# Kernel tuning notes

Hardware: AMD Instinct MI355X
Metric: run time of the kernel (lower is better)

The kernel has to match this reference:

```python
import math
import jax, jax.numpy as jnp
import numpy as np
from jax import lax

B, L = 8192, 512          # batch, seq_len; configs.d_model == seq_len (forced by LayerNorm over last dim)
TREND_POLY = 3
F_LEN = L // 2 - 1        # rfft bins after slicing [low_freq=1 : -1] for even t
TOP_K = int(math.log(F_LEN))  # = 5


def setup_inputs() -> dict:
    key = jax.random.key(0)
    ks = jax.random.split(key, 12)
    s = 0.02
    return {
        "x": jax.random.normal(ks[0], (B, L, 1), dtype=jnp.float32),
        "conv1_w": jax.random.normal(ks[1], (TREND_POLY, 1, 3), dtype=jnp.float32) * s,
        "conv1_b": jnp.zeros((TREND_POLY,), dtype=jnp.float32),
        "conv3_w": jax.random.normal(ks[2], (L, L, 3), dtype=jnp.float32) * s,
        "conv3_b": jnp.zeros((L,), dtype=jnp.float32),
        "w1": jax.random.normal(ks[3], (L, L), dtype=jnp.float32) * s,
        "b1": jnp.zeros((L,), dtype=jnp.float32),
        "w2": jax.random.normal(ks[4], (L, L), dtype=jnp.float32) * s,
        "b2": jnp.zeros((L,), dtype=jnp.float32),
        "ln_g": jnp.ones((L,), dtype=jnp.float32),
        "ln_b": jnp.zeros((L,), dtype=jnp.float32),
    }


def _gelu(x):
    return jax.nn.gelu(x, approximate=False)  # torch nn.GELU default (erf)


def _conv1d(x, w, b):
    # x: (b, Cin, T), w: (Cout, Cin, 3), padding=1
    y = lax.conv_general_dilated(x, w, window_strides=(1,), padding=[(1, 1)],
                                 dimension_numbers=("NCH", "OIH", "NCH"))
    return y + b[None, :, None]


def _trend_block(xp, conv1_w, conv1_b, conv3_w, conv3_b):
    # xp: (b, 1, L)
    h = _gelu(_conv1d(xp, conv1_w, conv1_b))        # (b, 3, L)
    h = h.transpose(0, 2, 1)                         # (b, L, 3) -- channels = seq_len
    h = _conv1d(h, conv3_w, conv3_b)                 # (b, L, 3)
    # poly_space: lin_space = [1/(out_dim+1)] = [0.5]; powers 1..3 -> (3, 1)
    lin = jnp.array([0.5], dtype=xp.dtype)
    poly = jnp.stack([lin ** (p + 1) for p in range(TREND_POLY)], axis=0)  # (3,1)
    # torch: (b,L,3) @ (3,1) -> (b,L,1) -> transpose -> (b,1,L)
    return jnp.einsum("blp,po->bol", h, poly)        # (b, 1, L)


def _fourier_layer(x):
    # x: (b, t, d=1); low_freq=1, t even
    b, t, d = x.shape
    xf = jnp.fft.rfft(x, axis=1)[:, 1:-1]            # (b, F, d) complex
    freqs = jnp.fft.rfftfreq(t).astype(x.dtype)[1:-1]  # (F,)
    mag = jnp.abs(xf)                                # (b, F, d)
    _, idx = lax.top_k(mag.transpose(0, 2, 1), TOP_K)  # (b, d, k)
    idx = idx.transpose(0, 2, 1)                     # (b, k, d)
    xf_sel = jnp.take_along_axis(xf, idx, axis=1)    # (b, k, d)
    f_sel = freqs[idx]                               # (b, k, d)
    # extrapolate with conjugate-symmetric pairs
    xf2 = jnp.concatenate([xf_sel, jnp.conj(xf_sel)], axis=1)       # (b, 2k, d)
    f2 = jnp.concatenate([f_sel, -f_sel], axis=1)[:, :, None, :]    # (b, 2k, 1, d)
    tt = jnp.arange(t, dtype=x.dtype)[None, None, :, None]          # (1, 1, t, 1)
    amp = jnp.abs(xf2)[:, :, None, :]                               # (b, 2k, 1, d)
    phase = jnp.arctan2(xf2.imag, xf2.real)[:, :, None, :]
    x_time = amp * jnp.cos(2.0 * math.pi * f2 * tt + phase)         # (b, 2k, t, d)
    return jnp.sum(x_time, axis=1)                                  # (b, t, d)


def reference(x, conv1_w, conv1_b, conv3_w, conv3_b, w1, b1, w2, b2, ln_g, ln_b):
    xp = x.transpose(0, 2, 1)                        # (b, 1, L)
    trend = _trend_block(xp, conv1_w, conv1_b, conv3_w, conv3_b)    # (b, 1, L)
    season = _fourier_layer(x).transpose(0, 2, 1)    # (b, 1, L)
    # residual MLP branch on enc_out = (b, 1, L); LayerNorm over last dim (== d_model)
    e = xp
    mu = jnp.mean(e, axis=-1, keepdims=True)
    var = jnp.mean((e - mu) ** 2, axis=-1, keepdims=True)
    ln = (e - mu) * lax.rsqrt(var + 1e-5) * ln_g + ln_b
    m = _gelu(jnp.einsum("bcl,ol->bco", ln, w1) + b1)
    m = jnp.einsum("bcl,ol->bco", m, w2) + b2        # dropout is identity at eval
    e = e + m
    mean = jnp.mean(e, axis=1, keepdims=True)        # dim 1 has size 1 -> mean == e
    return (e - mean, season, trend, mean)
```

## Files before the change

### kernel.cpp

```cpp
#include <hip/hip_runtime.h>
#include <hip/hip_bf16.h>
#include <math.h>

#define B_ 8192
#define L_ 512
#define BL_ (B_ * L_)
#define KT_ 1536

using bf16x8 = __attribute__((ext_vector_type(8))) short;
using f32x4  = __attribute__((ext_vector_type(4))) float;

__device__ __forceinline__ float gelu_f(float v) {
    return 0.5f * v * (1.0f + erff(v * 0.70710678118654752f));
}
__device__ __forceinline__ float bf2f(unsigned short u) {
    return __uint_as_float(((unsigned int)u) << 16);
}
__device__ __forceinline__ unsigned short f2bf(float f) {
    unsigned int x = __float_as_uint(f);
    x += 0x7fffu + ((x >> 16) & 1u);
    return (unsigned short)(x >> 16);
}
__device__ __forceinline__ void gload16(const void* g, void* l) {
    __builtin_amdgcn_global_load_lds(
        (const __attribute__((address_space(1))) unsigned int*)g,
        (__attribute__((address_space(3))) unsigned int*)l, 16, 0, 0);
}

__global__ __launch_bounds__(256) void k_fused_pre(const float* __restrict__ x,
        const float* __restrict__ c1w, const float* __restrict__ c1b,
        const float* __restrict__ lg, const float* __restrict__ lbias,
        unsigned short* __restrict__ h1, unsigned short* __restrict__ lnx,
        const float* __restrict__ c3w, const float* __restrict__ w1,
        const float* __restrict__ w2, unsigned short* __restrict__ weff,
        unsigned short* __restrict__ w1b, unsigned short* __restrict__ w2b,
        double2* __restrict__ tabd, float2* __restrict__ tab,
        float2* __restrict__ tab32) {
    const int tid = threadIdx.x;
    if (blockIdx.x >= B_) {
        int idx = (blockIdx.x - B_) * 256 + tid;
        if (idx < 512) {
            double sv, cv;
            sincos((double)idx * (3.14159265358979323846 / 256.0), &sv, &cv);
            tabd[idx] = make_double2(cv, sv);
            tab[idx] = make_float2((float)cv, (float)sv);
            if ((idx & 15) == 0) tab32[idx >> 4] = make_float2((float)cv, (float)sv);
        }
        int o = idx >> 9, i = idx & 511;
        const float* t = c3w + (size_t)idx * 3;
        float t0 = t[0], t1 = t[1], t2 = t[2];
        size_t base = (size_t)o * KT_ + i;
        weff[base]        = f2bf(0.25f * t0 + 0.5f * t1);
        weff[base + 512]  = f2bf(0.125f * t0 + 0.25f * t1 + 0.5f * t2);
        weff[base + 1024] = f2bf(0.125f * t1 + 0.25f * t2);
        w1b[idx] = f2bf(w1[idx]);
        w2b[idx] = f2bf(w2[idx]);
        return;
    }
    __shared__ float xs[512];
    __shared__ float red[8];
    const long b = blockIdx.x;
    const float* xr = x + (b << 9);
    float x0 = xr[tid], x1 = xr[tid + 256];
    xs[tid] = x0; xs[tid + 256] = x1;
    float s = x0 + x1, ss = x0 * x0 + x1 * x1;
#pragma unroll
    for (int off = 32; off > 0; off >>= 1) {
        s += __shfl_xor(s, off);
        ss += __shfl_xor(ss, off);
    }
    if ((tid & 63) == 0) { red[tid >> 6] = s; red[4 + (tid >> 6)] = ss; }
    __syncthreads();
    s  = red[0] + red[1] + red[2] + red[3];
    ss = red[4] + red[5] + red[6] + red[7];
    const float mu = s * (1.f / 512.f);
    const float rs = rsqrtf(ss * (1.f / 512.f) - mu * mu + 1e-5f);
    float w[9], cb[3];
#pragma unroll
    for (int j = 0; j < 9; ++j) w[j] = c1w[j];
#pragma unroll
    for (int j = 0; j < 3; ++j) cb[j] = c1b[j];
#pragma unroll
    for (int half = 0; half < 2; ++half) {
        const int i = tid + (half << 8);
        const float xm = i ? xs[i - 1] : 0.f;
        const float xc = xs[i];
        const float xp = (i != 511) ? xs[i + 1] : 0.f;
        unsigned short* hb = h1 + b * KT_ + i;
#pragma unroll
        for (int c = 0; c < 3; ++c) {
            float v = w[c * 3] * xm + w[c * 3 + 1] * xc + w[c * 3 + 2] * xp + cb[c];
            hb[(long)c << 9] = f2bf(gelu_f(v));
        }
        lnx[(b << 9) + i] = f2bf(fmaf((xc - mu) * rs, lg[i], lbias[i]));
    }
}

template<int EMODE, int KD>
__global__ __launch_bounds__(256) void k_mgemm(
        const unsigned short* __restrict__ A, const unsigned short* __restrict__ W,
        const float* __restrict__ bias, float sbias,
        const float* __restrict__ xres, void* __restrict__ Cp) {
    __shared__ short As[128][64];
    __shared__ short Bs[64][64];
    const int tid = threadIdx.x;
    const int lane = tid & 63;
    const int wid = tid >> 6;
    const int m0 = blockIdx.x << 7;
    const int n0 = blockIdx.y << 6;
    const int wm = (wid & 1) << 6;
    const int wn = (wid >> 1) << 5;
    f32x4 acc[4][2] = {};

    const int srow = tid >> 3;
    const int schunk = tid & 7;
    const unsigned short* Ab = A + (size_t)m0 * KD;
    const unsigned short* Wb = W + (size_t)n0 * KD;
    const int frow = lane & 15;
    const int fsw = frow & 7;
    const int s0 = lane >> 4;

    for (int k0 = 0; k0 < KD; k0 += 64) {
        __syncthreads();
#pragma unroll
        for (int seg = 0; seg < 4; ++seg) {
            const int r = (seg << 5) + srow;
            const int c = (schunk ^ (r & 7)) << 3;
            gload16(Ab + (size_t)r * KD + k0 + c, &As[r][schunk << 3]);
        }
#pragma unroll
        for (int seg = 0; seg < 2; ++seg) {
            const int r = (seg << 5) + srow;
            const int c = (schunk ^ (r & 7)) << 3;
            gload16(Wb + (size_t)r * KD + k0 + c, &Bs[r][schunk << 3]);
        }
        __syncthreads();
#pragma unroll
        for (int kk = 0; kk < 2; ++kk) {
            bf16x8 af[4], bfr[2];
            const int sl = (kk << 2) + s0;
#pragma unroll
            for (int m = 0; m < 4; ++m)
                af[m] = *(const bf16x8*)&As[wm + (m << 4) + frow][(sl ^ fsw) << 3];
#pragma unroll
            for (int n = 0; n < 2; ++n)
                bfr[n] = *(const bf16x8*)&Bs[wn + (n << 4) + frow][(sl ^ fsw) << 3];
#pragma unroll
            for (int m = 0; m < 4; ++m)
#pragma unroll
                for (int n = 0; n < 2; ++n)
                    acc[m][n] = __builtin_amdgcn_mfma_f32_16x16x32_bf16(af[m], bfr[n], acc[m][n], 0, 0, 0);
        }
    }

    const int col0 = n0 + wn + (lane & 15);
    const int rbase = m0 + wm + ((lane >> 4) << 2);
#pragma unroll
    for (int n = 0; n < 2; ++n) {
        const int col = col0 + (n << 4);
        const float bz = sbias * bias[col];
#pragma unroll
        for (int m = 0; m < 4; ++m) {
#pragma unroll
            for (int r = 0; r < 4; ++r) {
                const size_t row = rbase + (m << 4) + r;
                float v = acc[m][n][r] + bz;
                if (EMODE == 0) {
                    ((float*)Cp)[row * 512 + col] = v;
                } else if (EMODE == 1) {
                    ((unsigned short*)Cp)[row * 512 + col] = f2bf(gelu_f(v));
                } else {
                    ((float*)Cp)[row * 512 + col] = v + xres[row * 512 + col];
                }
            }
        }
    }
}

__global__ __launch_bounds__(256) void k_season(const float* __restrict__ x,
        const double2* __restrict__ gtabd, const float2* __restrict__ gtab,
        const float2* __restrict__ gtab32,
        float* __restrict__ out1, float* __restrict__ out0) {
    __shared__ float2 xp[2][256];
    __shared__ float2 tab[512];
    __shared__ float2 Ys[2][512];
    __shared__ unsigned long long wkey[2][4][5];
    __shared__ float2 wval[2][4][5];

    const int tid = threadIdx.x;
    const int w = tid >> 6, l = tid & 63;
    const long b = (long)blockIdx.x << 1;
    const float* xr0 = x + (b << 9);
    const float* xr1 = xr0 + 512;

    {
        const int t1s = tid >> 3, t0s = tid & 7;
        const int g = (t1s << 4) + t0s;
        xp[0][tid] = make_float2(xr0[g], xr0[g + 8]);
        xp[1][tid] = make_float2(xr1[g], xr1[g + 8]);
        tab[tid] = gtab[tid];
        tab[tid + 256] = gtab[tid + 256];
    }
    __syncthreads();

    const int rr = (w << 3) + (l & 7);
    const int t0 = l >> 3;
    float ra0 = 0.f, ia0 = 0.f, rb0 = 0.f, ib0 = 0.f;
    float ra1 = 0.f, ia1 = 0.f, rb1 = 0.f, ib1 = 0.f;
    int e32 = 0;
#pragma unroll
    for (int t1 = 0; t1 < 32; ++t1) {
        float2 wt = gtab32[e32];
        e32 = (e32 + rr) & 31;
        float2 v0 = xp[0][(t1 << 3) + t0];
        float2 v1 = xp[1][(t1 << 3) + t0];
        ra0 = fmaf(v0.x, wt.x, ra0); ia0 = fmaf(v0.x, wt.y, ia0);
        rb0 = fmaf(v0.y, wt.x, rb0); ib0 = fmaf(v0.y, wt.y, ib0);
        ra1 = fmaf(v1.x, wt.x, ra1); ia1 = fmaf(v1.x, wt.y, ia1);
        rb1 = fmaf(v1.y, wt.x, rb1); ib1 = fmaf(v1.y, wt.y, ib1);
    }
    Ys[0][(t0 << 5) + rr] = make_float2(ra0, -ia0);
    Ys[0][((t0 + 8) << 5) + rr] = make_float2(rb0, -ib0);
    Ys[1][(t0 << 5) + rr] = make_float2(ra1, -ia1);
    Ys[1][((t0 + 8) << 5) + rr] = make_float2(rb1, -ib1);

    const int k = ((l >> 3) << 5) + rr;
    double xre0 = 0.0, xim0 = 0.0, xre1 = 0.0, xim1 = 0.0;
    int e = 0;
#pragma unroll
    for (int t0i = 0; t0i < 16; ++t0i) {
        float2 y0 = Ys[0][(t0i << 5) + rr];
        float2 y1 = Ys[1][(t0i << 5) + rr];
        double2 wt = gtabd[e];
        e = (e + k) & 511;
        xre0 += (double)y0.x * wt.x + (double)y0.y * wt.y;
        xim0 += (double)y0.y * wt.x - (double)y0.x * wt.y;
        xre1 += (double)y1.x * wt.x + (double)y1.y * wt.y;
        xim1 += (double)y1.y * wt.x - (double)y1.x * wt.y;
    }

    unsigned long long key0 = 0, key1 = 0;
    if (k != 0) {
        double m0 = xre0 * xre0 + xim0 * xim0;
        double m1 = xre1 * xre1 + xim1 * xim1;
        key0 = (__double_as_longlong(m0) & ~0xFFFull) | (unsigned long long)(4095 - k);
        key1 = (__double_as_longlong(m1) & ~0xFFFull) | (unsigned long long)(4095 - k);
    }
    const float fre0 = (float)xre0, fim0 = (float)xim0;
    const float fre1 = (float)xre1, fim1 = (float)xim1;

    for (int rnd = 0; rnd < 5; ++rnd) {
        unsigned long long rk0 = key0, rk1 = key1;
#pragma unroll
        for (int off = 32; off > 0; off >>= 1) {
            unsigned long long o0 = __shfl_xor(rk0, off);
            unsigned long long o1 = __shfl_xor(rk1, off);
            rk0 = (o0 > rk0) ? o0 : rk0;
            rk1 = (o1 > rk1) ? o1 : rk1;
        }
        if (key0 == rk0 && rk0 != 0ull) {
            wkey[0][w][rnd] = rk0; wval[0][w][rnd] = make_float2(fre0, fim0); key0 = 0;
        }
        if (key1 == rk1 && rk1 != 0ull) {
            wkey[1][w][rnd] = rk1; wval[1][w][rnd] = make_float2(fre1, fim1); key1 = 0;
        }
    }
    __syncthreads();

#pragma unroll
    for (int row = 0; row < 2; ++row) {
        float4 sel[5];
        int h0 = 0, h1 = 0, h2 = 0, h3 = 0;
#pragma unroll
        for (int rnd = 0; rnd < 5; ++rnd) {
            unsigned long long c0 = wkey[row][0][h0], c1 = wkey[row][1][h1];
            unsigned long long c2 = wkey[row][2][h2], c3 = wkey[row][3][h3];
            unsigned long long bk = c0; int bw = 0;
            if (c1 > bk) { bk = c1; bw = 1; }
            if (c2 > bk) { bk = c2; bw = 2; }
            if (c3 > bk) { bk = c3; bw = 3; }
            const int hs = (bw == 0) ? h0 : (bw == 1) ? h1 : (bw == 2) ? h2 : h3;
            float2 v = wval[row][bw][hs];
            h0 += (bw == 0); h1 += (bw == 1); h2 += (bw == 2); h3 += (bw == 3);
            const int kk = 4095 - (int)(bk & 0xFFFull);
            sel[rnd] = make_float4((float)kk, v.x, v.y, 0.f);
        }
        const long ro = ((b + row) << 9);
#pragma unroll
        for (int half = 0; half < 2; ++half) {
            int t = tid + (half << 8);
            float acc = 0.f;
#pragma unroll
            for (int j = 0; j < 5; ++j) {
                float4 sj = sel[j];
                int kj = (int)sj.x;
                float2 wt = tab[(kj * t) & 511];
                acc += sj.y * wt.x - sj.z * wt.y;
            }
            out1[ro + t] = 2.f * acc;
            out0[ro + t] = 0.f;
        }
    }
}

extern "C" void kernel_launch(void* const* d_in, const int* in_sizes, int n_in,
                              void* d_out, int out_size, void* d_ws, size_t ws_size,
                              hipStream_t stream) {
    const float* x   = (const float*)d_in[0];
    const float* c1w = (const float*)d_in[1];
    const float* c1b = (const float*)d_in[2];
    const float* c3w = (const float*)d_in[3];
    const float* c3b = (const float*)d_in[4];
    const float* w1  = (const float*)d_in[5];
    const float* b1  = (const float*)d_in[6];
    const float* w2  = (const float*)d_in[7];
    const float* b2  = (const float*)d_in[8];
    const float* lg  = (const float*)d_in[9];
    const float* lb  = (const float*)d_in[10];

    float* out  = (float*)d_out;
    float* out1 = out + (long)BL_;
    float* out2 = out + 2L * BL_;
    float* out3 = out + 3L * BL_;

    double2* tabd = (double2*)d_ws;
    float2* tab   = (float2*)((char*)d_ws + 8192);
    float2* tab32 = (float2*)((char*)d_ws + 12288);

    unsigned short* h1   = (unsigned short*)d_out;
    unsigned short* weff = h1 + (size_t)B_ * KT_;
    unsigned short* w1b  = weff + (size_t)L_ * KT_;
    unsigned short* w2b  = w1b + (size_t)L_ * L_;
    unsigned short* lnx  = (unsigned short*)(out3);
    unsigned short* m1   = (unsigned short*)d_out;

    k_fused_pre<<<B_ + 1024, 256, 0, stream>>>(x, c1w, c1b, lg, lb, h1, lnx,
                                               c3w, w1, w2, weff, w1b, w2b,
                                               tabd, tab, tab32);
    k_mgemm<0, KT_><<<dim3(64, 8), 256, 0, stream>>>(h1, weff, c3b, 0.875f, nullptr, out2);
    k_mgemm<1, 512><<<dim3(64, 8), 256, 0, stream>>>(lnx, w1b, b1, 1.0f, nullptr, m1);
    k_mgemm<2, 512><<<dim3(64, 8), 256, 0, stream>>>(m1, w2b, b2, 1.0f, x, out3);
    k_season<<<B_ / 2, 256, 0, stream>>>(x, tabd, tab, tab32, out1, out);
}
```

Before: 115.5 us.

## Merge trend GEMM and first MLP GEMM into one launch using workspace buffer

When the workspace is large enough, the intermediate m1 moves into workspace, so the trend conv GEMM and the first MLP GEMM no longer alias and can run as one 1024-block launch. The zero-fill of output 0 moves from the season kernel into the second MLP GEMM epilogue. This cuts a launch and lets the two independent GEMMs fill the GPU together. The cost is runtime emode/KD branching in a shared device body instead of template specialization, which may hurt code quality. The block mix is also unbalanced, since K=1536 blocks run alongside K=512 blocks.

```diff
diff --git a/kernel.cpp b/kernel.cpp
--- a/kernel.cpp
+++ b/kernel.cpp
@@ -12,9 +12,6 @@
 
 __device__ __forceinline__ float gelu_f(float v) {
     return 0.5f * v * (1.0f + erff(v * 0.70710678118654752f));
-}
-__device__ __forceinline__ float bf2f(unsigned short u) {
-    return __uint_as_float(((unsigned int)u) << 16);
 }
 __device__ __forceinline__ unsigned short f2bf(float f) {
     unsigned int x = __float_as_uint(f);
@@ -96,18 +93,15 @@
     }
 }
 
-template<int EMODE, int KD>
-__global__ __launch_bounds__(256) void k_mgemm(
+__device__ __forceinline__ void gemm_body(
         const unsigned short* __restrict__ A, const unsigned short* __restrict__ W,
         const float* __restrict__ bias, float sbias,
-        const float* __restrict__ xres, void* __restrict__ Cp) {
-    __shared__ short As[128][64];
-    __shared__ short Bs[64][64];
+        const float* __restrict__ xres, float* __restrict__ out0z,
+        void* __restrict__ Cp, int KD, int emode, int m0, int n0,
+        short As[128][64], short Bs[64][64]) {
     const int tid = threadIdx.x;
     const int lane = tid & 63;
     const int wid = tid >> 6;
-    const int m0 = blockIdx.x << 7;
-    const int n0 = blockIdx.y << 6;
     const int wm = (wid & 1) << 6;
     const int wn = (wid >> 1) << 5;
     f32x4 acc[4][2] = {};
@@ -165,22 +159,53 @@
             for (int r = 0; r < 4; ++r) {
                 const size_t row = rbase + (m << 4) + r;
                 float v = acc[m][n][r] + bz;
-                if (EMODE == 0) {
+                if (emode == 0) {
                     ((float*)Cp)[row * 512 + col] = v;
-                } else if (EMODE == 1) {
+                } else if (emode == 1) {
                     ((unsigned short*)Cp)[row * 512 + col] = f2bf(gelu_f(v));
                 } else {
                     ((float*)Cp)[row * 512 + col] = v + xres[row * 512 + col];
+                    if (out0z) out0z[row * 512 + col] = 0.f;
                 }
             }
         }
+    }
+}
+
+template<int EMODE, int KD>
+__global__ __launch_bounds__(256) void k_mgemm(
+        const unsigned short* __restrict__ A, const unsigned short* __restrict__ W,
+        const float* __restrict__ bias, float sbias,
+        const float* __restrict__ xres, float* __restrict__ out0z,
+        void* __restrict__ Cp) {
+    __shared__ short As[128][64];
+    __shared__ short Bs[64][64];
+    gemm_body(A, W, bias, sbias, xres, out0z, Cp, KD, EMODE,
+              blockIdx.x << 7, blockIdx.y << 6, As, Bs);
+}
+
+__global__ __launch_bounds__(256) void k_mega(
+        const unsigned short* __restrict__ h1, const unsigned short* __restrict__ weff,
+        const float* __restrict__ c3b, float* __restrict__ out2,
+        const unsigned short* __restrict__ lnx, const unsigned short* __restrict__ w1b,
+        const float* __restrict__ b1, unsigned short* __restrict__ m1) {
+    __shared__ short As[128][64];
+    __shared__ short Bs[64][64];
+    int id = blockIdx.x;
+    if (id < 512) {
+        gemm_body(h1, weff, c3b, 0.875f, nullptr, nullptr, out2, KT_, 0,
+                  (id & 63) << 7, (id >> 6) << 6, As, Bs);
+    } else {
+        id -= 512;
+        gemm_body(lnx, w1b, b1, 1.0f, nullptr, nullptr, m1, 512, 1,
+                  (id & 63) << 7, (id >> 6) << 6, As, Bs);
     }
 }
 
 __global__ __launch_bounds__(256) void k_season(const float* __restrict__ x,
         const double2* __restrict__ gtabd, const float2* __restrict__ gtab,
         const float2* __restrict__ gtab32,
-        float* __restrict__ out1, float* __restrict__ out0) {
+        float* __restrict__ out1, float* __restrict__ out0z) {
     __shared__ float2 xp[2][256];
     __shared__ float2 tab[512];
     __shared__ float2 Ys[2][512];
@@ -298,7 +323,7 @@
                 acc += sj.y * wt.x - sj.z * wt.y;
             }
             out1[ro + t] = 2.f * acc;
-            out0[ro + t] = 0.f;
+            if (out0z) out0z[ro + t] = 0.f;
         }
     }
 }
@@ -326,19 +351,30 @@
     double2* tabd = (double2*)d_ws;
     float2* tab   = (float2*)((char*)d_ws + 8192);
     float2* tab32 = (float2*)((char*)d_ws + 12288);
+    const bool big_ws = ws_size >= (size_t)(16384 + 8 * 1024 * 1024);
 
     unsigned short* h1   = (unsigned short*)d_out;
     unsigned short* weff = h1 + (size_t)B_ * KT_;
     unsigned short* w1b  = weff + (size_t)L_ * KT_;
     unsigned short* w2b  = w1b + (size_t)L_ * L_;
     unsigned short* lnx  = (unsigned short*)(out3);
-    unsigned short* m1   = (unsigned short*)d_out;
 
     k_fused_pre<<<B_ + 1024, 256, 0, stream>>>(x, c1w, c1b, lg, lb, h1, lnx,
                                                c3w, w1, w2, weff, w1b, w2b,
                                                tabd, tab, tab32);
-    k_mgemm<0, KT_><<<dim3(64, 8), 256, 0, stream>>>(h1, weff, c3b, 0.875f, nullptr, out2);
-    k_mgemm<1, 512><<<dim3(64, 8), 256, 0, stream>>>(lnx, w1b, b1, 1.0f, nullptr, m1);
-    k_mgemm<2, 512><<<dim3(64, 8), 256, 0, stream>>>(m1, w2b, b2, 1.0f, x, out3);
-    k_season<<<B_ / 2, 256, 0, stream>>>(x, tabd, tab, tab32, out1, out);
-}
+    if (big_ws) {
+        unsigned short* m1 = (unsigned short*)((char*)d_ws + 16384);
+        k_mega<<<1024, 256, 0, stream>>>(h1, weff, c3b, out2, lnx, w1b, b1, m1);
+        k_mgemm<2, 512><<<dim3(64, 8), 256, 0, stream>>>(m1, w2b, b2, 1.0f, x, out, out3);
+        k_season<<<B_ / 2, 256, 0, stream>>>(x, tabd, tab, tab32, out1, nullptr);
+    } else {
+        unsigned short* m1 = (unsigned short*)d_out;
+        k_mgemm<0, KT_><<<dim3(64, 8), 256, 0, stream>>>(h1, weff, c3b, 0.875f,
+                                                         nullptr, nullptr, out2);
+        k_mgemm<1, 512><<<dim3(64, 8), 256, 0, stream>>>(lnx, w1b, b1, 1.0f,
+                                                         nullptr, nullptr, m1);
+        k_mgemm<2, 512><<<dim3(64, 8), 256, 0, stream>>>(m1, w2b, b2, 1.0f, x,
+                                                         nullptr, out3);
+        k_season<<<B_ / 2, 256, 0, stream>>>(x, tabd, tab, tab32, out1, out);
+    }
+}
```

Result: no change. 115.8 us (+0.3%).
